# Kernel tuning notes

Hardware: AMD Instinct MI355X
Metric: run time of the kernel (lower is better)

Reference implementation:

```python
import jax, jax.numpy as jnp
import numpy as np

K = 256
ALPHA = 0.2   # bml_alpha
BETA = 0.3    # bml_beta
EPS = 1e-8    # torch CosineSimilarity eps
NEG_INF = -10000.0
WEIGHT_TEMP = 0.05


def _l2n(x):
    # cosine-normalize rows, matching nn.CosineSimilarity's eps clamp
    n = jnp.linalg.norm(x, axis=-1, keepdims=True)
    return x / jnp.maximum(n, EPS)


def setup_inputs() -> dict:
    key = jax.random.key(0)
    k1, k2, k3 = jax.random.split(key, 3)
    B, D = 8192, 768
    datapoints = jax.random.normal(k1, (B, D), dtype=jnp.float32)
    centroid = jax.random.normal(k2, (K, D), dtype=jnp.float32)
    batch_cos_sim = jax.random.normal(k3, (B, B), dtype=jnp.float32)
    return {"datapoints": datapoints, "centroid": centroid, "batch_cos_sim": batch_cos_sim}


def reference(datapoints, centroid, batch_cos_sim):
    B = datapoints.shape[0]
    datapoints = jax.lax.stop_gradient(datapoints)  # forward() does clone().detach()

    # intra_cos_sim = cos(datapoints, centroid) / temp (temp=1)  -> [B, K]
    intra_cos_sim = _l2n(datapoints) @ _l2n(centroid).T

    # cluster assignment + intra-class adjacency
    dp_index = jnp.argmax(intra_cos_sim, axis=-1)                 # [B]
    onehot = jax.nn.one_hot(dp_index, K, dtype=jnp.float32)       # [B, K]
    dp_cluster = onehot @ onehot.T                                # [B, B]
    eye = jnp.eye(B, dtype=bool)
    dp_cluster = jnp.where(eye, 0.0, dp_cluster)                  # fill_diagonal_(0)

    # gather assigned centroid per datapoint
    dp_centroid = centroid[dp_index]                              # [B, D]

    # hard negative: 2nd-closest centroid (top-2 on cosine sim), detached
    _, top2_idx = jax.lax.top_k(intra_cos_sim, 2)                 # [B, 2]
    hard_negative = jax.lax.stop_gradient(centroid[top2_idx[:, 1]])  # [B, D]

    # false-negative BML loss on the in-batch cosine matrix
    pos = jnp.diagonal(batch_cos_sim)[:, None]                    # [B, 1]
    delta = (batch_cos_sim - pos) * dp_cluster                    # [B, B]
    fn_loss = (jax.nn.relu(delta + ALPHA) + jax.nn.relu(-delta - BETA)).mean()

    # softmax-weighted negatives (diag masked to -10000), detached
    masked = jnp.where(eye, NEG_INF, batch_cos_sim)
    weights = jax.lax.stop_gradient(jax.nn.softmax(masked, axis=-1) / WEIGHT_TEMP)

    return intra_cos_sim, dp_cluster, dp_centroid, hard_negative, fn_loss, weights
```

## Files before the change

### kernel.cpp

```cpp
#include <hip/hip_runtime.h>
#include <math.h>

#define B_N 8192
#define K_N 256
#define D_N 768
#define BM 32
#define KC 32

static constexpr float ALPHA_C = 0.2f;
static constexpr float BETA_C  = 0.3f;
static constexpr float EPS_C   = 1e-8f;
static constexpr float NEG_INF_C = -10000.0f;
static constexpr float INV_WTEMP = 20.0f;

__global__ __launch_bounds__(256) void k_centroid_prep(
        const float* __restrict__ centroid, float* __restrict__ cnt) {
    int c = blockIdx.x, t = threadIdx.x;
    const float* p = centroid + c * D_N;
    float v0 = p[t], v1 = p[t + 256], v2 = p[t + 512];
    float s = v0 * v0 + v1 * v1 + v2 * v2;
    #pragma unroll
    for (int o = 32; o >= 1; o >>= 1) s += __shfl_xor(s, o);
    __shared__ float red[4];
    __shared__ float sinv;
    if ((t & 63) == 0) red[t >> 6] = s;
    __syncthreads();
    if (t == 0)
        sinv = 1.0f / fmaxf(sqrtf(red[0] + red[1] + red[2] + red[3]), EPS_C);
    __syncthreads();
    float inv = sinv;
    cnt[(t)       * K_N + c] = v0 * inv;
    cnt[(t + 256) * K_N + c] = v1 * inv;
    cnt[(t + 512) * K_N + c] = v2 * inv;
}

__device__ __forceinline__ bool top_better(float v, int iv, float w, int iw) {
    return (v > w) || ((v == w) && (iv < iw));
}

__global__ __launch_bounds__(256) void k_intra(
        const float* __restrict__ dp, const float* __restrict__ cnt,
        const float* __restrict__ centroid,
        float* __restrict__ out_intra, unsigned char* __restrict__ cid_g,
        float* __restrict__ dp_centroid, float* __restrict__ hard_negative) {
    __shared__ float ct[KC][K_N];
    __shared__ float dpt[KC][BM + 4];
    __shared__ float sqp[BM][8];
    __shared__ float rn[BM];
    int t = threadIdx.x;
    int row0 = blockIdx.x * BM;
    int tx = t & 63, ty = t >> 6;
    int c0 = tx * 4;
    int r0 = ty * 8;
    int sr = t >> 3, skq = t & 7;

    float acc[8][4];
    #pragma unroll
    for (int r = 0; r < 8; ++r)
        #pragma unroll
        for (int c = 0; c < 4; ++c) acc[r][c] = 0.f;
    float ss = 0.f;

    for (int kb = 0; kb < D_N; kb += KC) {
        __syncthreads();
        #pragma unroll
        for (int u = 0; u < 8; ++u) {
            int f4 = t + 256 * u;
            int k = f4 >> 6, c4 = (f4 & 63) << 2;
            *(float4*)&ct[k][c4] = *(const float4*)&cnt[(size_t)(kb + k) * K_N + c4];
        }
        {
            float4 v = *(const float4*)&dp[(size_t)(row0 + sr) * D_N + kb + skq * 4];
            ss += v.x * v.x + v.y * v.y + v.z * v.z + v.w * v.w;
            dpt[skq * 4 + 0][sr] = v.x;
            dpt[skq * 4 + 1][sr] = v.y;
            dpt[skq * 4 + 2][sr] = v.z;
            dpt[skq * 4 + 3][sr] = v.w;
        }
        __syncthreads();
        #pragma unroll
        for (int k = 0; k < KC; ++k) {
            float4 b4 = *(float4*)&ct[k][c0];
            float4 a0 = *(float4*)&dpt[k][r0];
            float4 a1 = *(float4*)&dpt[k][r0 + 4];
            float a[8] = {a0.x, a0.y, a0.z, a0.w, a1.x, a1.y, a1.z, a1.w};
            float b[4] = {b4.x, b4.y, b4.z, b4.w};
            #pragma unroll
            for (int r = 0; r < 8; ++r)
                #pragma unroll
                for (int c = 0; c < 4; ++c)
                    acc[r][c] += a[r] * b[c];
        }
    }

    sqp[sr][skq] = ss;
    __syncthreads();
    if (t < BM) {
        float s = 0.f;
        #pragma unroll
        for (int j = 0; j < 8; ++j) s += sqp[t][j];
        rn[t] = 1.0f / fmaxf(sqrtf(s), EPS_C);
    }
    __syncthreads();

    #pragma unroll 1
    for (int r = 0; r < 8; ++r) {
        int row = row0 + r0 + r;
        float rv = rn[r0 + r];
        float4 o;
        o.x = acc[r][0] * rv; o.y = acc[r][1] * rv;
        o.z = acc[r][2] * rv; o.w = acc[r][3] * rv;
        *(float4*)&out_intra[(size_t)row * K_N + c0] = o;

        float m1 = o.x, m2 = -1e30f;
        int i1 = c0, i2 = K_N;
        { float v = o.y; int id = c0 + 1;
          if (v > m1) { m2 = m1; i2 = i1; m1 = v; i1 = id; } else if (v > m2) { m2 = v; i2 = id; } }
        { float v = o.z; int id = c0 + 2;
          if (v > m1) { m2 = m1; i2 = i1; m1 = v; i1 = id; } else if (v > m2) { m2 = v; i2 = id; } }
        { float v = o.w; int id = c0 + 3;
          if (v > m1) { m2 = m1; i2 = i1; m1 = v; i1 = id; } else if (v > m2) { m2 = v; i2 = id; } }
        #pragma unroll
        for (int off = 32; off >= 1; off >>= 1) {
            float om1 = __shfl_xor(m1, off);
            int   oi1 = __shfl_xor(i1, off);
            float om2 = __shfl_xor(m2, off);
            int   oi2 = __shfl_xor(i2, off);
            if (top_better(om1, oi1, m1, i1)) {
                if (top_better(m1, i1, om2, oi2)) { m2 = m1; i2 = i1; }
                else                              { m2 = om2; i2 = oi2; }
                m1 = om1; i1 = oi1;
            } else if (top_better(om1, oi1, m2, i2)) {
                m2 = om1; i2 = oi1;
            }
        }
        if (tx == 0) cid_g[row] = (unsigned char)i1;

        const float4* s1 = (const float4*)(centroid + (size_t)i1 * D_N);
        const float4* s2 = (const float4*)(centroid + (size_t)i2 * D_N);
        float4* d1 = (float4*)(dp_centroid   + (size_t)row * D_N);
        float4* d2 = (float4*)(hard_negative + (size_t)row * D_N);
        #pragma unroll
        for (int u = 0; u < 3; ++u) {
            d1[tx + 64 * u] = s1[tx + 64 * u];
            d2[tx + 64 * u] = s2[tx + 64 * u];
        }
    }
}

__global__ __launch_bounds__(256) void k_row(
        const float* __restrict__ bcs, const unsigned char* __restrict__ cid_g,
        float* __restrict__ dp_cluster, float* __restrict__ weights,
        double* __restrict__ accd) {
    int i = blockIdx.x;
    int t = threadIdx.x;
    __shared__ float4 row4[B_N / 4];
    __shared__ float  red[4];
    float* row = (float*)row4;
    const unsigned* cidw = (const unsigned*)cid_g;

    const float4* src = (const float4*)(bcs + (size_t)i * B_N);
    float mx = -3.0e38f;
    #pragma unroll
    for (int u = 0; u < 8; ++u) {
        int f4 = t + 256 * u;
        float4 v = src[f4];
        row4[f4] = v;
        int j0 = f4 * 4;
        float a = (j0     == i) ? NEG_INF_C : v.x;
        float b = (j0 + 1 == i) ? NEG_INF_C : v.y;
        float c = (j0 + 2 == i) ? NEG_INF_C : v.z;
        float d = (j0 + 3 == i) ? NEG_INF_C : v.w;
        mx = fmaxf(mx, fmaxf(fmaxf(a, b), fmaxf(c, d)));
    }
    __syncthreads();
    #pragma unroll
    for (int o = 32; o >= 1; o >>= 1) mx = fmaxf(mx, __shfl_xor(mx, o));
    if ((t & 63) == 0) red[t >> 6] = mx;
    __syncthreads();
    mx = fmaxf(fmaxf(red[0], red[1]), fmaxf(red[2], red[3]));

    float pos = row[i];
    unsigned myc = (unsigned)cid_g[i];
    __syncthreads();

    float fn = 0.f, se = 0.f;
    float* dcrow = dp_cluster + (size_t)i * B_N;
    #pragma unroll
    for (int r = 0; r < 8; ++r) {
        int f4 = t + 256 * r;
        int j0 = f4 * 4;
        unsigned cw = cidw[f4];
        float4 v = row4[f4];
        float4 e, dc;
        {
            bool same = ((cw & 255u) == myc) & (j0 != i);
            float delta = same ? (v.x - pos) : 0.f;
            fn += fmaxf(delta + ALPHA_C, 0.f) + fmaxf(-delta - BETA_C, 0.f);
            dc.x = same ? 1.0f : 0.f;
            e.x = __expf(((j0 == i) ? NEG_INF_C : v.x) - mx);
        }
        {
            bool same = (((cw >> 8) & 255u) == myc) & (j0 + 1 != i);
            float delta = same ? (v.y - pos) : 0.f;
            fn += fmaxf(delta + ALPHA_C, 0.f) + fmaxf(-delta - BETA_C, 0.f);
            dc.y = same ? 1.0f : 0.f;
            e.y = __expf(((j0 + 1 == i) ? NEG_INF_C : v.y) - mx);
        }
        {
            bool same = (((cw >> 16) & 255u) == myc) & (j0 + 2 != i);
            float delta = same ? (v.z - pos) : 0.f;
            fn += fmaxf(delta + ALPHA_C, 0.f) + fmaxf(-delta - BETA_C, 0.f);
            dc.z = same ? 1.0f : 0.f;
            e.z = __expf(((j0 + 2 == i) ? NEG_INF_C : v.z) - mx);
        }
        {
            bool same = (((cw >> 24) & 255u) == myc) & (j0 + 3 != i);
            float delta = same ? (v.w - pos) : 0.f;
            fn += fmaxf(delta + ALPHA_C, 0.f) + fmaxf(-delta - BETA_C, 0.f);
            dc.w = same ? 1.0f : 0.f;
            e.w = __expf(((j0 + 3 == i) ? NEG_INF_C : v.w) - mx);
        }
        se += e.x + e.y + e.z + e.w;
        row4[f4] = e;
        ((float4*)dcrow)[f4] = dc;
    }

    #pragma unroll
    for (int o = 32; o >= 1; o >>= 1) se += __shfl_xor(se, o);
    if ((t & 63) == 0) red[t >> 6] = se;
    __syncthreads();
    se = red[0] + red[1] + red[2] + red[3];
    float inv = INV_WTEMP / se;

    float* wrow = weights + (size_t)i * B_N;
    #pragma unroll
    for (int r = 0; r < 32; ++r) {
        int j = t + 256 * r;
        wrow[j] = row[j] * inv;
    }

    #pragma unroll
    for (int o = 32; o >= 1; o >>= 1) fn += __shfl_xor(fn, o);
    __syncthreads();
    if ((t & 63) == 0) red[t >> 6] = fn;
    __syncthreads();
    if (t == 0) atomicAdd(accd, (double)(red[0] + red[1] + red[2] + red[3]));
}

__global__ void k_final(const double* __restrict__ acc, float* __restrict__ out) {
    out[0] = (float)(acc[0] / ((double)B_N * (double)B_N));
}

extern "C" void kernel_launch(void* const* d_in, const int* in_sizes, int n_in,
                              void* d_out, int out_size, void* d_ws, size_t ws_size,
                              hipStream_t stream) {
    const float* dp       = (const float*)d_in[0];
    const float* centroid = (const float*)d_in[1];
    const float* bcs      = (const float*)d_in[2];
    float* out = (float*)d_out;

    float* intra       = out;
    float* dp_cluster  = out + 2097152;
    float* dp_centroid = out + 69206016;
    float* hard_neg    = out + 75497472;
    float* fn_out      = out + 81788928;
    float* weights     = out + 81788929;

    char* ws = (char*)d_ws;
    double*        acc = (double*)ws;
    float*         cnt = (float*)(ws + 256);
    unsigned char* cid = (unsigned char*)(ws + 256 + 786432);

    hipMemsetAsync(ws, 0, 16, stream);
    k_centroid_prep<<<K_N, 256, 0, stream>>>(centroid, cnt);
    k_intra<<<B_N / BM, 256, 0, stream>>>(dp, cnt, centroid, intra, cid,
                                          dp_centroid, hard_neg);
    k_row<<<B_N, 256, 0, stream>>>(bcs, cid, dp_cluster, weights, acc);
    k_final<<<1, 1, 0, stream>>>(acc, fn_out);
}
```

Baseline: 242.5 us.

## Register-prefetch centroid tiles, broadcast datapoints via readlane, keep softmax rows in registers

In the intra-similarity GEMM, the next centroid tile and datapoint slice are prefetched into registers while the current tile is computed. Datapoint values are broadcast across the wave with readlane instead of being staged transposed in shared memory, and row norms come from a shuffle reduction. The row kernel now keeps its 32 values per thread in registers instead of a shared-memory row buffer and uses scalar strided accesses. This cuts shared-memory traffic and LDS footprint, at the cost of higher register pressure and narrower (non-float4) global loads and stores in the row kernel.

```diff
diff --git a/kernel.cpp b/kernel.cpp
--- a/kernel.cpp
+++ b/kernel.cpp
@@ -6,12 +6,17 @@
 #define D_N 768
 #define BM 32
 #define KC 32
+#define NKB (D_N / KC)
 
 static constexpr float ALPHA_C = 0.2f;
 static constexpr float BETA_C  = 0.3f;
 static constexpr float EPS_C   = 1e-8f;
 static constexpr float NEG_INF_C = -10000.0f;
 static constexpr float INV_WTEMP = 20.0f;
+
+__device__ __forceinline__ float rdlane(float x, int l) {
+    return __int_as_float(__builtin_amdgcn_readlane(__float_as_int(x), l));
+}
 
 __global__ __launch_bounds__(256) void k_centroid_prep(
         const float* __restrict__ centroid, float* __restrict__ cnt) {
@@ -44,69 +49,74 @@
         float* __restrict__ out_intra, unsigned char* __restrict__ cid_g,
         float* __restrict__ dp_centroid, float* __restrict__ hard_negative) {
     __shared__ float ct[KC][K_N];
-    __shared__ float dpt[KC][BM + 4];
-    __shared__ float sqp[BM][8];
-    __shared__ float rn[BM];
     int t = threadIdx.x;
+    int l = t & 63;
+    int ty = t >> 6;
     int row0 = blockIdx.x * BM;
-    int tx = t & 63, ty = t >> 6;
-    int c0 = tx * 4;
+    int c0 = l * 4;
     int r0 = ty * 8;
-    int sr = t >> 3, skq = t & 7;
+    int myrow = row0 + r0 + (l >> 3);
+    int kq = l & 7;
+    int sk = t >> 6;
 
     float acc[8][4];
     #pragma unroll
     for (int r = 0; r < 8; ++r)
         #pragma unroll
         for (int c = 0; c < 4; ++c) acc[r][c] = 0.f;
+
+    float4 sreg[8];
+    #pragma unroll
+    for (int u = 0; u < 8; ++u)
+        sreg[u] = *(const float4*)&cnt[(size_t)(sk + 4 * u) * K_N + c0];
+    float4 dcur = *(const float4*)&dp[(size_t)myrow * D_N + kq * 4];
+    #pragma unroll
+    for (int u = 0; u < 8; ++u)
+        *(float4*)&ct[sk + 4 * u][c0] = sreg[u];
+    __syncthreads();
+
     float ss = 0.f;
-
-    for (int kb = 0; kb < D_N; kb += KC) {
-        __syncthreads();
-        #pragma unroll
-        for (int u = 0; u < 8; ++u) {
-            int f4 = t + 256 * u;
-            int k = f4 >> 6, c4 = (f4 & 63) << 2;
-            *(float4*)&ct[k][c4] = *(const float4*)&cnt[(size_t)(kb + k) * K_N + c4];
-        }
-        {
-            float4 v = *(const float4*)&dp[(size_t)(row0 + sr) * D_N + kb + skq * 4];
-            ss += v.x * v.x + v.y * v.y + v.z * v.z + v.w * v.w;
-            dpt[skq * 4 + 0][sr] = v.x;
-            dpt[skq * 4 + 1][sr] = v.y;
-            dpt[skq * 4 + 2][sr] = v.z;
-            dpt[skq * 4 + 3][sr] = v.w;
-        }
-        __syncthreads();
+    for (int kbi = 0; kbi < NKB; ++kbi) {
+        int kbn = (kbi + 1 < NKB) ? (kbi + 1) * KC : 0;
+        #pragma unroll
+        for (int u = 0; u < 8; ++u)
+            sreg[u] = *(const float4*)&cnt[(size_t)(kbn + sk + 4 * u) * K_N + c0];
+        float4 dnxt = *(const float4*)&dp[(size_t)myrow * D_N + kbn + kq * 4];
+
+        ss += dcur.x * dcur.x + dcur.y * dcur.y + dcur.z * dcur.z + dcur.w * dcur.w;
+
         #pragma unroll
         for (int k = 0; k < KC; ++k) {
             float4 b4 = *(float4*)&ct[k][c0];
-            float4 a0 = *(float4*)&dpt[k][r0];
-            float4 a1 = *(float4*)&dpt[k][r0 + 4];
-            float a[8] = {a0.x, a0.y, a0.z, a0.w, a1.x, a1.y, a1.z, a1.w};
-            float b[4] = {b4.x, b4.y, b4.z, b4.w};
+            float comp = ((k & 3) == 0) ? dcur.x : ((k & 3) == 1) ? dcur.y
+                       : ((k & 3) == 2) ? dcur.z : dcur.w;
             #pragma unroll
-            for (int r = 0; r < 8; ++r)
-                #pragma unroll
-                for (int c = 0; c < 4; ++c)
-                    acc[r][c] += a[r] * b[c];
-        }
-    }
-
-    sqp[sr][skq] = ss;
-    __syncthreads();
-    if (t < BM) {
-        float s = 0.f;
-        #pragma unroll
-        for (int j = 0; j < 8; ++j) s += sqp[t][j];
-        rn[t] = 1.0f / fmaxf(sqrtf(s), EPS_C);
-    }
-    __syncthreads();
+            for (int r = 0; r < 8; ++r) {
+                float a = rdlane(comp, (r << 3) | (k >> 2));
+                acc[r][0] += a * b4.x;
+                acc[r][1] += a * b4.y;
+                acc[r][2] += a * b4.z;
+                acc[r][3] += a * b4.w;
+            }
+        }
+        __syncthreads();
+        if (kbi + 1 < NKB) {
+            #pragma unroll
+            for (int u = 0; u < 8; ++u)
+                *(float4*)&ct[sk + 4 * u][c0] = sreg[u];
+        }
+        dcur = dnxt;
+        __syncthreads();
+    }
+
+    #pragma unroll
+    for (int o = 1; o <= 4; o <<= 1) ss += __shfl_xor(ss, o);
+    float rinv = 1.0f / fmaxf(sqrtf(ss), EPS_C);
 
     #pragma unroll 1
     for (int r = 0; r < 8; ++r) {
         int row = row0 + r0 + r;
-        float rv = rn[r0 + r];
+        float rv = rdlane(rinv, r << 3);
         float4 o;
         o.x = acc[r][0] * rv; o.y = acc[r][1] * rv;
         o.z = acc[r][2] * rv; o.w = acc[r][3] * rv;
@@ -134,7 +144,7 @@
                 m2 = om1; i2 = oi1;
             }
         }
-        if (tx == 0) cid_g[row] = (unsigned char)i1;
+        if (l == 0) cid_g[row] = (unsigned char)i1;
 
         const float4* s1 = (const float4*)(centroid + (size_t)i1 * D_N);
         const float4* s2 = (const float4*)(centroid + (size_t)i2 * D_N);
@@ -142,8 +152,8 @@
         float4* d2 = (float4*)(hard_negative + (size_t)row * D_N);
         #pragma unroll
         for (int u = 0; u < 3; ++u) {
-            d1[tx + 64 * u] = s1[tx + 64 * u];
-            d2[tx + 64 * u] = s2[tx + 64 * u];
+            d1[l + 64 * u] = s1[l + 64 * u];
+            d2[l + 64 * u] = s2[l + 64 * u];
         }
     }
 }
@@ -154,76 +164,40 @@
         double* __restrict__ accd) {
     int i = blockIdx.x;
     int t = threadIdx.x;
-    __shared__ float4 row4[B_N / 4];
-    __shared__ float  red[4];
-    float* row = (float*)row4;
-    const unsigned* cidw = (const unsigned*)cid_g;
-
-    const float4* src = (const float4*)(bcs + (size_t)i * B_N);
+    __shared__ float red[4];
+    __shared__ float posb;
+
+    const float* src = bcs + (size_t)i * B_N;
+    float v[32];
     float mx = -3.0e38f;
     #pragma unroll
-    for (int u = 0; u < 8; ++u) {
-        int f4 = t + 256 * u;
-        float4 v = src[f4];
-        row4[f4] = v;
-        int j0 = f4 * 4;
-        float a = (j0     == i) ? NEG_INF_C : v.x;
-        float b = (j0 + 1 == i) ? NEG_INF_C : v.y;
-        float c = (j0 + 2 == i) ? NEG_INF_C : v.z;
-        float d = (j0 + 3 == i) ? NEG_INF_C : v.w;
-        mx = fmaxf(mx, fmaxf(fmaxf(a, b), fmaxf(c, d)));
-    }
-    __syncthreads();
+    for (int u = 0; u < 32; ++u) {
+        int j = t + 256 * u;
+        v[u] = src[j];
+        if (j == i) posb = v[u];
+        mx = fmaxf(mx, (j == i) ? NEG_INF_C : v[u]);
+    }
     #pragma unroll
     for (int o = 32; o >= 1; o >>= 1) mx = fmaxf(mx, __shfl_xor(mx, o));
     if ((t & 63) == 0) red[t >> 6] = mx;
     __syncthreads();
     mx = fmaxf(fmaxf(red[0], red[1]), fmaxf(red[2], red[3]));
-
-    float pos = row[i];
+    float pos = posb;
     unsigned myc = (unsigned)cid_g[i];
     __syncthreads();
 
     float fn = 0.f, se = 0.f;
     float* dcrow = dp_cluster + (size_t)i * B_N;
     #pragma unroll
-    for (int r = 0; r < 8; ++r) {
-        int f4 = t + 256 * r;
-        int j0 = f4 * 4;
-        unsigned cw = cidw[f4];
-        float4 v = row4[f4];
-        float4 e, dc;
-        {
-            bool same = ((cw & 255u) == myc) & (j0 != i);
-            float delta = same ? (v.x - pos) : 0.f;
-            fn += fmaxf(delta + ALPHA_C, 0.f) + fmaxf(-delta - BETA_C, 0.f);
-            dc.x = same ? 1.0f : 0.f;
-            e.x = __expf(((j0 == i) ? NEG_INF_C : v.x) - mx);
-        }
-        {
-            bool same = (((cw >> 8) & 255u) == myc) & (j0 + 1 != i);
-            float delta = same ? (v.y - pos) : 0.f;
-            fn += fmaxf(delta + ALPHA_C, 0.f) + fmaxf(-delta - BETA_C, 0.f);
-            dc.y = same ? 1.0f : 0.f;
-            e.y = __expf(((j0 + 1 == i) ? NEG_INF_C : v.y) - mx);
-        }
-        {
-            bool same = (((cw >> 16) & 255u) == myc) & (j0 + 2 != i);
-            float delta = same ? (v.z - pos) : 0.f;
-            fn += fmaxf(delta + ALPHA_C, 0.f) + fmaxf(-delta - BETA_C, 0.f);
-            dc.z = same ? 1.0f : 0.f;
-            e.z = __expf(((j0 + 2 == i) ? NEG_INF_C : v.z) - mx);
-        }
-        {
-            bool same = (((cw >> 24) & 255u) == myc) & (j0 + 3 != i);
-            float delta = same ? (v.w - pos) : 0.f;
-            fn += fmaxf(delta + ALPHA_C, 0.f) + fmaxf(-delta - BETA_C, 0.f);
-            dc.w = same ? 1.0f : 0.f;
-            e.w = __expf(((j0 + 3 == i) ? NEG_INF_C : v.w) - mx);
-        }
-        se += e.x + e.y + e.z + e.w;
-        row4[f4] = e;
-        ((float4*)dcrow)[f4] = dc;
+    for (int u = 0; u < 32; ++u) {
+        int j = t + 256 * u;
+        bool same = ((unsigned)cid_g[j] == myc) & (j != i);
+        float delta = same ? (v[u] - pos) : 0.f;
+        fn += fmaxf(delta + ALPHA_C, 0.f) + fmaxf(-delta - BETA_C, 0.f);
+        dcrow[j] = same ? 1.0f : 0.f;
+        float e = __expf(((j == i) ? NEG_INF_C : v[u]) - mx);
+        se += e;
+        v[u] = e;
     }
 
     #pragma unroll
@@ -235,10 +209,8 @@
 
     float* wrow = weights + (size_t)i * B_N;
     #pragma unroll
-    for (int r = 0; r < 32; ++r) {
-        int j = t + 256 * r;
-        wrow[j] = row[j] * inv;
-    }
+    for (int u = 0; u < 32; ++u)
+        wrow[t + 256 * u] = v[u] * inv;
 
     #pragma unroll
     for (int o = 32; o >= 1; o >>= 1) fn += __shfl_xor(fn, o);
```

Measured after the change: 464.7 us. +91.6%, slower.

## Prefetch centroid tiles via registers and broadcast datapoint values with readlane

Applied to the files above, without the earlier changes.

The k_intra GEMM loop is restructured. The next centroid tile and datapoint chunk are loaded into registers while the current tile is being computed, giving a software pipeline. The datapoint shared-memory tile is removed: each wave holds its own 8 rows in registers and broadcasts values with v_readlane, and row norms are reduced with wave shuffles instead of shared memory. This cuts LDS traffic and exposes more load latency hiding, at the cost of more registers and many scalar readlane instructions in the inner loop.

```diff
diff --git a/kernel.cpp b/kernel.cpp
--- a/kernel.cpp
+++ b/kernel.cpp
@@ -6,12 +6,17 @@
 #define D_N 768
 #define BM 32
 #define KC 32
+#define NKB (D_N / KC)
 
 static constexpr float ALPHA_C = 0.2f;
 static constexpr float BETA_C  = 0.3f;
 static constexpr float EPS_C   = 1e-8f;
 static constexpr float NEG_INF_C = -10000.0f;
 static constexpr float INV_WTEMP = 20.0f;
+
+__device__ __forceinline__ float rdlane(float x, int l) {
+    return __int_as_float(__builtin_amdgcn_readlane(__float_as_int(x), l));
+}
 
 __global__ __launch_bounds__(256) void k_centroid_prep(
         const float* __restrict__ centroid, float* __restrict__ cnt) {
@@ -44,69 +49,74 @@
         float* __restrict__ out_intra, unsigned char* __restrict__ cid_g,
         float* __restrict__ dp_centroid, float* __restrict__ hard_negative) {
     __shared__ float ct[KC][K_N];
-    __shared__ float dpt[KC][BM + 4];
-    __shared__ float sqp[BM][8];
-    __shared__ float rn[BM];
     int t = threadIdx.x;
+    int l = t & 63;
+    int ty = t >> 6;
     int row0 = blockIdx.x * BM;
-    int tx = t & 63, ty = t >> 6;
-    int c0 = tx * 4;
+    int c0 = l * 4;
     int r0 = ty * 8;
-    int sr = t >> 3, skq = t & 7;
+    int myrow = row0 + r0 + (l >> 3);
+    int kq = l & 7;
+    int sk = ty;
 
     float acc[8][4];
     #pragma unroll
     for (int r = 0; r < 8; ++r)
         #pragma unroll
         for (int c = 0; c < 4; ++c) acc[r][c] = 0.f;
+
+    float4 sreg[8];
+    #pragma unroll
+    for (int u = 0; u < 8; ++u)
+        sreg[u] = *(const float4*)&cnt[(size_t)(sk + 4 * u) * K_N + c0];
+    float4 dcur = *(const float4*)&dp[(size_t)myrow * D_N + kq * 4];
+    #pragma unroll
+    for (int u = 0; u < 8; ++u)
+        *(float4*)&ct[sk + 4 * u][c0] = sreg[u];
+    __syncthreads();
+
     float ss = 0.f;
-
-    for (int kb = 0; kb < D_N; kb += KC) {
-        __syncthreads();
-        #pragma unroll
-        for (int u = 0; u < 8; ++u) {
-            int f4 = t + 256 * u;
-            int k = f4 >> 6, c4 = (f4 & 63) << 2;
-            *(float4*)&ct[k][c4] = *(const float4*)&cnt[(size_t)(kb + k) * K_N + c4];
-        }
-        {
-            float4 v = *(const float4*)&dp[(size_t)(row0 + sr) * D_N + kb + skq * 4];
-            ss += v.x * v.x + v.y * v.y + v.z * v.z + v.w * v.w;
-            dpt[skq * 4 + 0][sr] = v.x;
-            dpt[skq * 4 + 1][sr] = v.y;
-            dpt[skq * 4 + 2][sr] = v.z;
-            dpt[skq * 4 + 3][sr] = v.w;
-        }
-        __syncthreads();
+    for (int kbi = 0; kbi < NKB; ++kbi) {
+        int kbn = (kbi + 1 < NKB) ? (kbi + 1) * KC : 0;
+        #pragma unroll
+        for (int u = 0; u < 8; ++u)
+            sreg[u] = *(const float4*)&cnt[(size_t)(kbn + sk + 4 * u) * K_N + c0];
+        float4 dnxt = *(const float4*)&dp[(size_t)myrow * D_N + kbn + kq * 4];
+
+        ss += dcur.x * dcur.x + dcur.y * dcur.y + dcur.z * dcur.z + dcur.w * dcur.w;
+
         #pragma unroll
         for (int k = 0; k < KC; ++k) {
             float4 b4 = *(float4*)&ct[k][c0];
-            float4 a0 = *(float4*)&dpt[k][r0];
-            float4 a1 = *(float4*)&dpt[k][r0 + 4];
-            float a[8] = {a0.x, a0.y, a0.z, a0.w, a1.x, a1.y, a1.z, a1.w};
-            float b[4] = {b4.x, b4.y, b4.z, b4.w};
+            float comp = ((k & 3) == 0) ? dcur.x : ((k & 3) == 1) ? dcur.y
+                       : ((k & 3) == 2) ? dcur.z : dcur.w;
             #pragma unroll
-            for (int r = 0; r < 8; ++r)
-                #pragma unroll
-                for (int c = 0; c < 4; ++c)
-                    acc[r][c] += a[r] * b[c];
-        }
-    }
-
-    sqp[sr][skq] = ss;
-    __syncthreads();
-    if (t < BM) {
-        float s = 0.f;
-        #pragma unroll
-        for (int j = 0; j < 8; ++j) s += sqp[t][j];
-        rn[t] = 1.0f / fmaxf(sqrtf(s), EPS_C);
-    }
-    __syncthreads();
+            for (int r = 0; r < 8; ++r) {
+                float a = rdlane(comp, (r << 3) | (k >> 2));
+                acc[r][0] += a * b4.x;
+                acc[r][1] += a * b4.y;
+                acc[r][2] += a * b4.z;
+                acc[r][3] += a * b4.w;
+            }
+        }
+        __syncthreads();
+        if (kbi + 1 < NKB) {
+            #pragma unroll
+            for (int u = 0; u < 8; ++u)
+                *(float4*)&ct[sk + 4 * u][c0] = sreg[u];
+        }
+        dcur = dnxt;
+        __syncthreads();
+    }
+
+    #pragma unroll
+    for (int o = 1; o <= 4; o <<= 1) ss += __shfl_xor(ss, o);
+    float rinv = 1.0f / fmaxf(sqrtf(ss), EPS_C);
 
     #pragma unroll 1
     for (int r = 0; r < 8; ++r) {
         int row = row0 + r0 + r;
-        float rv = rn[r0 + r];
+        float rv = rdlane(rinv, r << 3);
         float4 o;
         o.x = acc[r][0] * rv; o.y = acc[r][1] * rv;
         o.z = acc[r][2] * rv; o.w = acc[r][3] * rv;
@@ -134,7 +144,7 @@
                 m2 = om1; i2 = oi1;
             }
         }
-        if (tx == 0) cid_g[row] = (unsigned char)i1;
+        if (l == 0) cid_g[row] = (unsigned char)i1;
 
         const float4* s1 = (const float4*)(centroid + (size_t)i1 * D_N);
         const float4* s2 = (const float4*)(centroid + (size_t)i2 * D_N);
@@ -142,8 +152,8 @@
         float4* d2 = (float4*)(hard_negative + (size_t)row * D_N);
         #pragma unroll
         for (int u = 0; u < 3; ++u) {
-            d1[tx + 64 * u] = s1[tx + 64 * u];
-            d2[tx + 64 * u] = s2[tx + 64 * u];
+            d1[l + 64 * u] = s1[l + 64 * u];
+            d2[l + 64 * u] = s2[l + 64 * u];
         }
     }
 }
```

Result: slower. 344.8 us (+42.2%).
